# Kernel tuning notes

Hardware: AMD Instinct MI355X
Metric: run time of the kernel (lower is better)

## Reference

```python
import jax, jax.numpy as jnp
import numpy as np

B, L, H, NH = 32, 200, 64, 2
HS = H // NH
NEG = -2.0**32 + 1.0  # matches torch paddings = -2**32 + 1


def _split_heads(x):
    # torch: cat(split(x, HS, dim=2), dim=0) -> [(h b) l d], head varies slowest
    b, l, _ = x.shape
    return x.reshape(b, l, NH, HS).transpose(2, 0, 1, 3).reshape(NH * b, l, HS)


def setup_inputs() -> dict:
    key = jax.random.key(0)
    ks = jax.random.split(key, 12)
    s = 1.0 / np.sqrt(H)
    return {
        "queries": jax.random.normal(ks[0], (B, L, H), jnp.float32),
        "keys": jax.random.normal(ks[1], (B, L, H), jnp.float32),
        "values": jax.random.normal(ks[2], (B, L, H), jnp.float32),
        "time_matrix_K": jax.random.normal(ks[3], (NH * B, L, L, H), jnp.float32),
        "time_mask": jax.random.bernoulli(ks[4], 0.1, (B, L)),  # True = padded query position
        "attn_mask": jnp.triu(jnp.ones((L, L), bool), k=1),      # True = masked (causal)
        "Wq": jax.random.normal(ks[5], (H, H), jnp.float32) * s,
        "bq": jnp.zeros((H,), jnp.float32),
        "Wk": jax.random.normal(ks[6], (H, H), jnp.float32) * s,
        "bk": jnp.zeros((H,), jnp.float32),
        "Wv": jax.random.normal(ks[7], (H, H), jnp.float32) * s,
        "bv": jnp.zeros((H,), jnp.float32),
        "Wt": jax.random.normal(ks[8], (H, H), jnp.float32) * s,
        "bt": jnp.zeros((H,), jnp.float32),
        "Wp": jax.random.normal(ks[9], (H, 1), jnp.float32) * s,
        "bp": jnp.zeros((1,), jnp.float32),
    }


def reference(queries, keys, values, time_matrix_K, time_mask, attn_mask,
              Wq, bq, Wk, bk, Wv, bv, Wt, bt, Wp, bp):
    Q = queries @ Wq + bq
    K = keys @ Wk + bk
    V = values @ Wv + bv
    Q_ = _split_heads(Q)   # [hB, L, HS]
    K_ = _split_heads(K)
    V_ = _split_heads(V)

    attn = jnp.einsum('bqd,bkd->bqk', Q_, K_)  # [hB, L, L]
    # time bias: Linear -> ReLU -> Linear(->1) -> sigmoid -> squeeze
    tw = jax.nn.sigmoid((jax.nn.relu(time_matrix_K @ Wt + bt) @ Wp + bp)[..., 0])  # [hB, L, L]
    # note: log-bias added BEFORE scaling, as in the original
    attn = (attn + jnp.log(tw)) / jnp.sqrt(jnp.asarray(HS, attn.dtype))

    tm = jnp.tile(time_mask, (NH, 1))[:, :, None]      # [hB, L, 1] -> broadcast over keys
    mask = tm | attn_mask[None, :, :]                  # [hB, L, L]
    attn = jnp.where(mask, jnp.asarray(NEG, attn.dtype), attn)
    attn = jax.nn.softmax(attn, axis=-1)
    # dropout is identity in eval/deterministic mode

    out = jnp.einsum('bqk,bkd->bqd', attn, V_)         # [hB, L, HS]
    # torch: cat(split(out, B, dim=0), dim=2) -> [B, L, H]
    out = out.reshape(NH, B, L, HS).transpose(1, 2, 0, 3).reshape(B, L, H)
    return out, attn
```

## Files before the change

kernel.cpp:

```cpp
#include <hip/hip_runtime.h>
#include <math.h>

#define BB 32
#define LL 200
#define HH 64
#define HSS 32
#define HB 64
#define TRI (LL*(LL+1)/2)
#define NEGV (-4294967295.0f)

typedef __bf16 bf16x8 __attribute__((ext_vector_type(8)));
typedef float f32x4 __attribute__((ext_vector_type(4)));

__global__ __launch_bounds__(64) void proj_kernel(
    const float* __restrict__ q_in, const float* __restrict__ k_in,
    const float* __restrict__ v_in,
    const float* __restrict__ Wq, const float* __restrict__ bq,
    const float* __restrict__ Wk, const float* __restrict__ bk,
    const float* __restrict__ Wv, const float* __restrict__ bv,
    float* __restrict__ Qs, float* __restrict__ Ks, float* __restrict__ Vs)
{
    const int row = blockIdx.x;
    const int b = row / LL, l = row % LL;
    const int j = threadIdx.x;

    __shared__ float s[3][HH];
    s[0][j] = q_in[row*HH + j];
    s[1][j] = k_in[row*HH + j];
    s[2][j] = v_in[row*HH + j];
    __syncthreads();

    const float* W[3]    = {Wq, Wk, Wv};
    const float* bias[3] = {bq, bk, bv};
    float*       dst[3]  = {Qs, Ks, Vs};

    const int hb  = (j >> 5)*BB + b;
    const int idx = (hb*LL + l)*HSS + (j & 31);

    #pragma unroll
    for (int m = 0; m < 3; ++m) {
        float acc = bias[m][j];
        #pragma unroll
        for (int i = 0; i < HH; ++i)
            acc = fmaf(s[m][i], W[m][i*HH + j], acc);
        dst[m][idx] = acc;
    }
}

__global__ __launch_bounds__(256) void prep_kernel(
    const float* __restrict__ Wt, unsigned short* __restrict__ WtT)
{
    const int t = blockIdx.x*256 + threadIdx.x;
    if (t < HH*HH) {
        const int n = t >> 6, k = t & 63;
        const __bf16 h = (__bf16)Wt[k*HH + n];
        WtT[t] = __builtin_bit_cast(unsigned short, h);
    }
}

__global__ __launch_bounds__(256) void mlp_kernel(
    const float* __restrict__ T,
    const unsigned short* __restrict__ WtT,
    const float* __restrict__ bt, const float* __restrict__ Wp,
    float* __restrict__ Plog)
{
    const int hb   = blockIdx.y;
    const int r0   = blockIdx.x * 256;
    const int tid  = threadIdx.x;
    const int wave = tid >> 6;
    const int lane = tid & 63;
    const int bl   = lane & 15;
    const int bg   = lane >> 4;

    __shared__ __align__(16) unsigned short sA[2][64*HH];
    __shared__ int sBase[256];

    {
        int r = r0 + tid; if (r >= TRI) r = TRI - 1;
        const float s = sqrtf((float)(8*r + 1));
        int qq = (int)((s - 1.0f) * 0.5f);
        while ((qq + 1)*(qq + 2)/2 <= r) ++qq;
        while (qq*(qq + 1)/2 > r) --qq;
        const int kk = r - qq*(qq + 1)/2;
        sBase[tid] = ((hb*LL + qq)*LL + kk) << 4;
    }
    __syncthreads();

    const float4* T4 = reinterpret_cast<const float4*>(T);

#define LOADCHUNK(CUR, c)                                                      \
    {                                                                          \
        _Pragma("unroll")                                                      \
        for (int i = 0; i < 4; ++i) {                                          \
            const int g = i*256 + tid;                                         \
            CUR[i] = T4[sBase[(c)*64 + (g >> 4)] + (g & 15)];                  \
        }                                                                      \
    }

    float4 va[4], vb[4];
    LOADCHUNK(va, 0)
    LOADCHUNK(vb, 1)

    bf16x8 bfrag[4][2];
    float  btv[4], wpv[4];
    #pragma unroll
    for (int n = 0; n < 4; ++n) {
        #pragma unroll
        for (int k = 0; k < 2; ++k) {
            const uint4 raw = *reinterpret_cast<const uint4*>(
                WtT + ((n*16 + bl)*HH + k*32 + bg*8));
            bfrag[n][k] = __builtin_bit_cast(bf16x8, raw);
        }
        btv[n] = bt[n*16 + bl];
        wpv[n] = Wp[n*16 + bl];
    }

#define PACK_ISSUE_COMPUTE(c, CUR, DO_ISSUE, NC)                               \
    {                                                                          \
                     \
        _Pragma("unroll")                                                      \
        for (int i = 0; i < 4; ++i) {                                          \
            const int g = i*256 + tid;                                         \
            const int row = g >> 4, cf4 = g & 15;                              \
            union { __bf16 h[4]; uint2 u2; } pk;                               \
            pk.h[0] = (__bf16)CUR[i].x; pk.h[1] = (__bf16)CUR[i].y;            \
            pk.h[2] = (__bf16)CUR[i].z; pk.h[3] = (__bf16)CUR[i].w;            \
            const int byteoff = row*128 + ((cf4*8) ^ ((row & 7) << 4));        \
            *reinterpret_cast<uint2*>(                                         \
                reinterpret_cast<char*>(sA[(c) & 1]) + byteoff) = pk.u2;       \
        }                                                                      \
        if (DO_ISSUE) LOADCHUNK(CUR, NC)          \
           \
        asm volatile("s_waitcnt lgkmcnt(0)" ::: "memory");                     \
        __builtin_amdgcn_s_barrier();                                          \
                                                                               \
        const int arow = wave*16 + bl;                                         \
        bf16x8 afrag[2];                                                       \
        _Pragma("unroll")                                                      \
        for (int k = 0; k < 2; ++k) {                                          \
            const int abyte = arow*128 + ((k*64 + bg*16) ^ ((arow & 7) << 4)); \
            const uint4 raw = *reinterpret_cast<const uint4*>(                 \
                reinterpret_cast<const char*>(sA[(c) & 1]) + abyte);           \
            afrag[k] = __builtin_bit_cast(bf16x8, raw);                        \
        }                                                                      \
        f32x4 acc[4];                                                          \
        _Pragma("unroll")                                                      \
        for (int n = 0; n < 4; ++n) {                                          \
            acc[n] = (f32x4){0.f, 0.f, 0.f, 0.f};                              \
            acc[n] = __builtin_amdgcn_mfma_f32_16x16x32_bf16(                  \
                         afrag[0], bfrag[n][0], acc[n], 0, 0, 0);              \
            acc[n] = __builtin_amdgcn_mfma_f32_16x16x32_bf16(                  \
                         afrag[1], bfrag[n][1], acc[n], 0, 0, 0);              \
        }                                                                      \
        float p[4] = {0.f, 0.f, 0.f, 0.f};                                     \
        _Pragma("unroll")                                                      \
        for (int n = 0; n < 4; ++n) {                                          \
            _Pragma("unroll")                                                  \
            for (int r = 0; r < 4; ++r)                                        \
                p[r] = fmaf(fmaxf(acc[n][r] + btv[n], 0.f), wpv[n], p[r]);     \
        }                                                                      \
        _Pragma("unroll")                                                      \
        for (int m = 1; m < 16; m <<= 1) {                                     \
            _Pragma("unroll")                                                  \
            for (int r = 0; r < 4; ++r) p[r] += __shfl_xor(p[r], m, 64);       \
        }                                                                      \
        if (bl == 0) {                                                         \
            _Pragma("unroll")                                                  \
            for (int r = 0; r < 4; ++r) {                                      \
                const int lr = (c)*64 + wave*16 + bg*4 + r;                    \
                if (r0 + lr < TRI)                                             \
                    Plog[sBase[lr] >> 4] = p[r];       \
            }                                                                  \
        }                                                                      \
    }

    PACK_ISSUE_COMPUTE(0, va, 1, 2)
    PACK_ISSUE_COMPUTE(1, vb, 1, 3)
    PACK_ISSUE_COMPUTE(2, va, 0, 0)
    PACK_ISSUE_COMPUTE(3, vb, 0, 0)
#undef PACK_ISSUE_COMPUTE
#undef LOADCHUNK
}

__global__ __launch_bounds__(256) void attn2_kernel(
    const float* __restrict__ Qs, const float* __restrict__ Ks,
    const float* __restrict__ Vs,
    const int*   __restrict__ time_mask,
    const float* __restrict__ bp,
    float* __restrict__ out, float* __restrict__ attn_out )
{
    const int q    = blockIdx.x;
    const int hb   = blockIdx.y;
    const int b    = hb & (BB-1);
    const int head = hb >> 5;
    const int tid  = threadIdx.x;
    const int wave = tid >> 6;
    const int lane = tid & 63;

    __shared__ float sQ[HSS];
    __shared__ float sLogit[LL];
    __shared__ float sRed[8];
    __shared__ float sO[8][HSS];

    if (tid < HSS) sQ[tid] = Qs[(hb*LL + q)*HSS + tid];
    const bool qmask = (time_mask[b*LL + q] != 0);
    const float bp0 = bp[0];
    const float scale = 0.17677669529663687f;
    __syncthreads();

    if (tid < LL) {
        float logit = NEGV;
        if (!qmask && tid <= q) {
            const float4* kr = reinterpret_cast<const float4*>(
                Ks + (hb*LL + tid)*HSS);
            float qk = 0.0f;
            #pragma unroll
            for (int i = 0; i < 8; ++i) {
                const float4 kv = kr[i];
                qk += kv.x*sQ[4*i+0] + kv.y*sQ[4*i+1]
                    + kv.z*sQ[4*i+2] + kv.w*sQ[4*i+3];
            }
            const float p  = attn_out[((size_t)hb*LL + q)*LL + tid];
            const float x  = p + bp0;
            const float ls = -logf(1.0f + expf(-x));
            logit = (qk + ls) * scale;
        }
        sLogit[tid] = logit;
    }
    __syncthreads();

    const float v = (tid < LL) ? sLogit[tid] : -INFINITY;
    float mx = v;
    #pragma unroll
    for (int s = 1; s < 64; s <<= 1) mx = fmaxf(mx, __shfl_xor(mx, s, 64));
    if (lane == 0) sRed[wave] = mx;
    __syncthreads();
    const float rowmax = fmaxf(fmaxf(sRed[0], sRed[1]), fmaxf(sRed[2], sRed[3]));

    const float e = (tid < LL) ? expf(v - rowmax) : 0.0f;
    float sm = e;
    #pragma unroll
    for (int s = 1; s < 64; s <<= 1) sm += __shfl_xor(sm, s, 64);
    if (lane == 0) sRed[4 + wave] = sm;
    __syncthreads();
    const float rowsum = sRed[4] + sRed[5] + sRed[6] + sRed[7];
    const float a = e * (1.0f / rowsum);

    __syncthreads();
    if (tid < LL) {
        sLogit[tid] = a;
        attn_out[((size_t)hb*LL + q)*LL + tid] = a;
    }
    __syncthreads();

    {
        const int d = tid & 31;
        const int g = tid >> 5;
        float acc = 0.0f;
        for (int k = g*25; k < g*25 + 25; ++k)
            acc = fmaf(sLogit[k], Vs[(hb*LL + k)*HSS + d], acc);
        sO[g][d] = acc;
        __syncthreads();
        if (tid < HSS) {
            float o = 0.0f;
            #pragma unroll
            for (int g2 = 0; g2 < 8; ++g2) o += sO[g2][tid];
            out[((size_t)b*LL + q)*HH + head*HSS + tid] = o;
        }
    }
}

extern "C" void kernel_launch(void* const* d_in, const int* in_sizes, int n_in,
                              void* d_out, int out_size, void* d_ws, size_t ws_size,
                              hipStream_t stream) {
    const float* queries = (const float*)d_in[0];
    const float* keys    = (const float*)d_in[1];
    const float* values  = (const float*)d_in[2];
    const float* T       = (const float*)d_in[3];
    const int*   tmask   = (const int*)d_in[4];
    const float* Wq = (const float*)d_in[6];
    const float* bq = (const float*)d_in[7];
    const float* Wk = (const float*)d_in[8];
    const float* bk = (const float*)d_in[9];
    const float* Wv = (const float*)d_in[10];
    const float* bv = (const float*)d_in[11];
    const float* Wt = (const float*)d_in[12];
    const float* bt = (const float*)d_in[13];
    const float* Wp = (const float*)d_in[14];
    const float* bp = (const float*)d_in[15];

    float* Qs = (float*)d_ws;
    float* Ks = Qs + HB*LL*HSS;
    float* Vs = Ks + HB*LL*HSS;
    unsigned short* WtT = (unsigned short*)(Vs + HB*LL*HSS);

    float* out      = (float*)d_out;
    float* attn_out = out + BB*LL*HH;

    prep_kernel<<<16, 256, 0, stream>>>(Wt, WtT);
    proj_kernel<<<BB*LL, 64, 0, stream>>>(queries, keys, values,
                                          Wq, bq, Wk, bk, Wv, bv,
                                          Qs, Ks, Vs);

    dim3 mgrid((TRI + 255) / 256, HB);
    mlp_kernel<<<mgrid, 256, 0, stream>>>(T, WtT, bt, Wp, attn_out);

    dim3 agrid(LL, HB);
    attn2_kernel<<<agrid, 256, 0, stream>>>(Qs, Ks, Vs, tmask, bp,
                                            out, attn_out);
}
```

Baseline: 123.7 us.

## Fold weight prep into projection, double MLP rows per block, hoist attn load

Removes the separate prep_kernel launch by having the first 64 blocks of proj_kernel write the transposed bf16 Wt. Each mlp_kernel block now handles 512 triangle rows instead of 256, running eight pipelined chunks so index and setup work is spread over more rows and fewer blocks launch. In attn2_kernel the per-key MLP logit load is issued before the first barrier so its latency overlaps the Q load. The risks are fewer MLP blocks, which lowers parallelism, and the extra branch added to proj_kernel.

```diff
diff --git a/kernel.cpp b/kernel.cpp
--- a/kernel.cpp
+++ b/kernel.cpp
@@ -7,6 +7,7 @@
 #define HSS 32
 #define HB 64
 #define TRI (LL*(LL+1)/2)
+#define ROWS 512
 #define NEGV (-4294967295.0f)
 
 typedef __bf16 bf16x8 __attribute__((ext_vector_type(8)));
@@ -18,11 +19,19 @@
     const float* __restrict__ Wq, const float* __restrict__ bq,
     const float* __restrict__ Wk, const float* __restrict__ bk,
     const float* __restrict__ Wv, const float* __restrict__ bv,
+    const float* __restrict__ Wt, unsigned short* __restrict__ WtT,
     float* __restrict__ Qs, float* __restrict__ Ks, float* __restrict__ Vs)
 {
     const int row = blockIdx.x;
     const int b = row / LL, l = row % LL;
     const int j = threadIdx.x;
+
+    if (blockIdx.x < 64) {
+        const int t = blockIdx.x*64 + j;
+        const int n = t >> 6, k = t & 63;
+        const __bf16 h = (__bf16)Wt[k*HH + n];
+        WtT[t] = __builtin_bit_cast(unsigned short, h);
+    }
 
     __shared__ float s[3][HH];
     s[0][j] = q_in[row*HH + j];
@@ -44,17 +53,6 @@
         for (int i = 0; i < HH; ++i)
             acc = fmaf(s[m][i], W[m][i*HH + j], acc);
         dst[m][idx] = acc;
-    }
-}
-
-__global__ __launch_bounds__(256) void prep_kernel(
-    const float* __restrict__ Wt, unsigned short* __restrict__ WtT)
-{
-    const int t = blockIdx.x*256 + threadIdx.x;
-    if (t < HH*HH) {
-        const int n = t >> 6, k = t & 63;
-        const __bf16 h = (__bf16)Wt[k*HH + n];
-        WtT[t] = __builtin_bit_cast(unsigned short, h);
     }
 }
 
@@ -65,7 +63,7 @@
     float* __restrict__ Plog)
 {
     const int hb   = blockIdx.y;
-    const int r0   = blockIdx.x * 256;
+    const int r0   = blockIdx.x * ROWS;
     const int tid  = threadIdx.x;
     const int wave = tid >> 6;
     const int lane = tid & 63;
@@ -73,16 +71,18 @@
     const int bg   = lane >> 4;
 
     __shared__ __align__(16) unsigned short sA[2][64*HH];
-    __shared__ int sBase[256];
-
-    {
-        int r = r0 + tid; if (r >= TRI) r = TRI - 1;
+    __shared__ int sBase[ROWS];
+
+    #pragma unroll
+    for (int j = 0; j < ROWS/256; ++j) {
+        int r = r0 + j*256 + tid;
+        if (r >= TRI) r = TRI - 1;
         const float s = sqrtf((float)(8*r + 1));
         int qq = (int)((s - 1.0f) * 0.5f);
         while ((qq + 1)*(qq + 2)/2 <= r) ++qq;
         while (qq*(qq + 1)/2 > r) --qq;
         const int kk = r - qq*(qq + 1)/2;
-        sBase[tid] = ((hb*LL + qq)*LL + kk) << 4;
+        sBase[j*256 + tid] = ((hb*LL + qq)*LL + kk) << 4;
     }
     __syncthreads();
 
@@ -176,8 +176,12 @@
 
     PACK_ISSUE_COMPUTE(0, va, 1, 2)
     PACK_ISSUE_COMPUTE(1, vb, 1, 3)
-    PACK_ISSUE_COMPUTE(2, va, 0, 0)
-    PACK_ISSUE_COMPUTE(3, vb, 0, 0)
+    PACK_ISSUE_COMPUTE(2, va, 1, 4)
+    PACK_ISSUE_COMPUTE(3, vb, 1, 5)
+    PACK_ISSUE_COMPUTE(4, va, 1, 6)
+    PACK_ISSUE_COMPUTE(5, vb, 1, 7)
+    PACK_ISSUE_COMPUTE(6, va, 0, 0)
+    PACK_ISSUE_COMPUTE(7, vb, 0, 0)
 #undef PACK_ISSUE_COMPUTE
 #undef LOADCHUNK
 }
@@ -202,15 +206,20 @@
     __shared__ float sRed[8];
     __shared__ float sO[8][HSS];
 
+    const bool qmask = (time_mask[b*LL + q] != 0);
+    const bool live  = (tid < LL) && !qmask && (tid <= q);
+
+    float pv = 0.0f;
+    if (live) pv = attn_out[((size_t)hb*LL + q)*LL + tid];
+
     if (tid < HSS) sQ[tid] = Qs[(hb*LL + q)*HSS + tid];
-    const bool qmask = (time_mask[b*LL + q] != 0);
     const float bp0 = bp[0];
     const float scale = 0.17677669529663687f;
     __syncthreads();
 
     if (tid < LL) {
         float logit = NEGV;
-        if (!qmask && tid <= q) {
+        if (live) {
             const float4* kr = reinterpret_cast<const float4*>(
                 Ks + (hb*LL + tid)*HSS);
             float qk = 0.0f;
@@ -220,8 +229,7 @@
                 qk += kv.x*sQ[4*i+0] + kv.y*sQ[4*i+1]
                     + kv.z*sQ[4*i+2] + kv.w*sQ[4*i+3];
             }
-            const float p  = attn_out[((size_t)hb*LL + q)*LL + tid];
-            const float x  = p + bp0;
+            const float x  = pv + bp0;
             const float ls = -logf(1.0f + expf(-x));
             logit = (qk + ls) * scale;
         }
@@ -297,12 +305,11 @@
     float* out      = (float*)d_out;
     float* attn_out = out + BB*LL*HH;
 
-    prep_kernel<<<16, 256, 0, stream>>>(Wt, WtT);
     proj_kernel<<<BB*LL, 64, 0, stream>>>(queries, keys, values,
                                           Wq, bq, Wk, bk, Wv, bv,
-                                          Qs, Ks, Vs);
-
-    dim3 mgrid((TRI + 255) / 256, HB);
+                                          Wt, WtT, Qs, Ks, Vs);
+
+    dim3 mgrid((TRI + ROWS - 1) / ROWS, HB);
     mlp_kernel<<<mgrid, 256, 0, stream>>>(T, WtT, bt, Wp, attn_out);
 
     dim3 agrid(LL, HB);
```

Result: faster. 119.5 us (-3.4%).
